# Kernel optimization log

Measured on AMD Instinct MI355X. Metric: run time of the kernel, lower is better.

Reference implementation:

```python
import jax, jax.numpy as jnp
import numpy as np

N_FFT = 2048
HOP = 441
WIN_SIZE = 7
PAD = WIN_SIZE // 2
NP_WIN = WIN_SIZE * WIN_SIZE
COV_NORM = NP_WIN / (NP_WIN - 1.0)  # sample covariance, skimage default
DATA_RANGE = 2.0  # skimage float dtype_range (-1,1)
C1 = (0.01 * DATA_RANGE) ** 2
C2 = (0.03 * DATA_RANGE) ** 2
EPS = 1e-8

# periodic hann window (librosa fftbins=True)
_HANN = 0.5 - 0.5 * np.cos(2.0 * np.pi * np.arange(N_FFT) / N_FFT)


def wav_to_spectrogram(x):
    # x: [B, C, S] -> magnitude spectrogram [B, C, T, F]
    pad = N_FFT // 2
    xp = jnp.pad(x, ((0, 0), (0, 0), (pad, pad)), mode='reflect')  # torch 'reflect'
    L = xp.shape[-1]
    n_frames = (L - N_FFT) // HOP + 1
    idx = jnp.arange(n_frames)[:, None] * HOP + jnp.arange(N_FFT)[None, :]
    frames = xp[..., idx] * jnp.asarray(_HANN, xp.dtype)  # [B,C,T,N_FFT]
    spec = jnp.fft.rfft(frames, axis=-1)
    mag = jnp.sqrt(jnp.maximum(spec.real ** 2 + spec.imag ** 2, EPS))
    return mag


def _umean_last(x):
    # 1D uniform mean filter (size 7) along last axis, scipy 'reflect' boundary
    xp = jnp.pad(x, [(0, 0)] * (x.ndim - 1) + [(PAD, PAD)], mode='symmetric')
    cs = jnp.cumsum(xp, axis=-1)
    zero = jnp.zeros(cs.shape[:-1] + (1,), cs.dtype)
    cs = jnp.concatenate([zero, cs], axis=-1)
    return (cs[..., WIN_SIZE:] - cs[..., :-WIN_SIZE]) / WIN_SIZE


def umean2d(x):
    # separable 7x7 uniform filter over last two axes
    x = _umean_last(x)
    x = jnp.swapaxes(_umean_last(jnp.swapaxes(x, -1, -2)), -1, -2)
    return x


def ssim_map_mean(X, Y):
    ux, uy = umean2d(X), umean2d(Y)
    uxx, uyy, uxy = umean2d(X * X), umean2d(Y * Y), umean2d(X * Y)
    vx = COV_NORM * (uxx - ux * ux)
    vy = COV_NORM * (uyy - uy * uy)
    vxy = COV_NORM * (uxy - ux * uy)
    S = ((2 * ux * uy + C1) * (2 * vxy + C2)) / ((ux * ux + uy * uy + C1) * (vx + vy + C2))
    # crop pad on each side (skimage) then mean over the spatial map
    return jnp.mean(S[..., PAD:-PAD, PAD:-PAD], axis=(-2, -1))


def setup_inputs() -> dict:
    key = jax.random.key(0)
    k1, k2 = jax.random.split(key)
    B, C, S = 32, 2, 176400
    output = jax.random.normal(k1, (B, C, S), dtype=jnp.float32)
    target = jax.random.normal(k2, (B, C, S), dtype=jnp.float32)
    return {"output": output, "target": target}


def reference(output, target):
    so = wav_to_spectrogram(output)
    st = wav_to_spectrogram(target)
    res = ssim_map_mean(so, st)  # [B, C]
    return res[..., None, None]  # [B, C, 1, 1]
```

## Files before the change

kernel.cpp:

```cpp
#include <hip/hip_runtime.h>
#include <math.h>

#ifndef M_PI
#define M_PI 3.14159265358979323846
#endif

constexpr int S_LEN    = 176400;
constexpr int NFFT     = 2048;
constexpr int NC       = 1024;
constexpr int HOP_     = 441;
constexpr int T_FRAMES = 401;
constexpr int F_BINS   = 1025;
constexpr int F_STRIDE = 1028;
constexpr int N_CH     = 64;
constexpr float EPS_   = 1e-8f;
constexpr float C1_    = 0.0004f;
constexpr float C2_    = 0.0036f;
constexpr float COV_NORM_ = 49.0f / 48.0f;

constexpr int WINP_OFF = 0;
constexpr int TG1_OFF  = 2048;
constexpr int TG2_OFF  = 4096;
constexpr int UTW_OFF  = 4224;
constexpr int SPEC_OFF = 6400;
constexpr int RPB_     = 10;
constexpr int N_CHUNKS = 40;

#define WAVE_SYNC() asm volatile("s_waitcnt lgkmcnt(0)" ::: "memory")

__device__ __forceinline__ float2 cadd(float2 a, float2 b){ return make_float2(a.x+b.x, a.y+b.y); }
__device__ __forceinline__ float2 csub(float2 a, float2 b){ return make_float2(a.x-b.x, a.y-b.y); }
__device__ __forceinline__ float2 cmul(float2 a, float2 b){ return make_float2(a.x*b.x-a.y*b.y, a.x*b.y+a.y*b.x); }
__device__ __forceinline__ float2 mulnegi(float2 v){ return make_float2(v.y, -v.x); }

__device__ __constant__ float2 W16C[10] = {
    { 1.0f, 0.0f},
    { 0.92387953251128674f, -0.38268343236508978f},
    { 0.70710678118654752f, -0.70710678118654752f},
    { 0.38268343236508978f, -0.92387953251128674f},
    { 0.0f, -1.0f},
    {-0.38268343236508978f, -0.92387953251128674f},
    {-0.70710678118654752f, -0.70710678118654752f},
    {-0.92387953251128674f, -0.38268343236508978f},
    {-1.0f, 0.0f},
    {-0.92387953251128674f,  0.38268343236508978f},
};

__device__ __forceinline__ void fft16(float2 (&r)[16]) {
    float2 C[4][4];
    #pragma unroll
    for (int m2 = 0; m2 < 4; ++m2) {
        float2 u0 = r[m2], u1 = r[4+m2], u2 = r[8+m2], u3 = r[12+m2];
        float2 t0 = cadd(u0,u2), t1 = csub(u0,u2), t2 = cadd(u1,u3), t3 = csub(u1,u3);
        C[0][m2] = cadd(t0,t2);
        C[1][m2] = cadd(t1, mulnegi(t3));
        C[2][m2] = csub(t0,t2);
        C[3][m2] = csub(t1, mulnegi(t3));
    }
    #pragma unroll
    for (int a = 0; a < 4; ++a) {
        float2 u0 = C[a][0];
        float2 u1 = (a == 0) ? C[a][1] : cmul(C[a][1], W16C[a]);
        float2 u2 = (a == 0) ? C[a][2] : cmul(C[a][2], W16C[2*a]);
        float2 u3 = (a == 0) ? C[a][3] : cmul(C[a][3], W16C[3*a]);
        float2 t0 = cadd(u0,u2), t1 = csub(u0,u2), t2 = cadd(u1,u3), t3 = csub(u1,u3);
        r[a]      = cadd(t0,t2);
        r[a+4]    = cadd(t1, mulnegi(t3));
        r[a+8]    = csub(t0,t2);
        r[a+12]   = csub(t1, mulnegi(t3));
    }
}

__global__ __launch_bounds__(256) void init_tables_kernel(float* __restrict__ ws, float* __restrict__ out) {
    const int idx = blockIdx.x * 256 + threadIdx.x;
    if (idx < 64) out[idx] = 0.0f;
    if (idx < 1024) {
        float w0 = 0.5f - 0.5f * cosf((float)(2.0 * M_PI / NFFT) * (float)(2*idx));
        float w1 = 0.5f - 0.5f * cosf((float)(2.0 * M_PI / NFFT) * (float)(2*idx+1));
        ws[WINP_OFF + 2*idx]   = w0;
        ws[WINP_OFF + 2*idx+1] = w1;
    }
    if (idx < 1024) {
        int k1 = idx >> 6, L = idx & 63;
        float ang = -2.0f * (float)M_PI * (float)(L * k1) / (float)NC;
        float s, c; sincosf(ang, &s, &c);
        ws[TG1_OFF + 2*idx] = c; ws[TG1_OFF + 2*idx+1] = s;
    }
    if (idx < 64) {
        int k2 = idx >> 2, n3 = idx & 3;
        float ang = -2.0f * (float)M_PI * (float)(n3 * k2) / 64.0f;
        float s, c; sincosf(ang, &s, &c);
        ws[TG2_OFF + 2*idx] = c; ws[TG2_OFF + 2*idx+1] = s;
    }
    if (idx < F_BINS) {
        float ang = -(float)M_PI * (float)idx / (float)NC;
        float s, c; sincosf(ang, &s, &c);
        ws[UTW_OFF + 2*idx] = c; ws[UTW_OFF + 2*idx+1] = s;
    }
}

__global__ __launch_bounds__(256) void stft_mag_kernel(
    const float* __restrict__ x0, const float* __restrict__ x1,
    float* __restrict__ ws, int ch0, int nch, int swizzle)
{
    __shared__ float2 lds[4][1024];

    const int tid  = threadIdx.x;
    const int wave = tid >> 6;
    const int L    = tid & 63;

    int ch, pair;
    if (swizzle) {
        int g = blockIdx.x;
        int xcd = g & 7;
        int s = g >> 3;
        int cl = s & 7;
        pair = s >> 3;
        ch = ch0 + xcd * 8 + cl;
    } else {
        pair = blockIdx.x;
        ch = ch0 + blockIdx.y;
    }
    const int which = wave >> 1;
    const int t = 2 * pair + (wave & 1);
    if (t > 400) return;

    const float* __restrict__ xin = (which ? x1 : x0) + (size_t)ch * S_LEN;
    const float2* __restrict__ winp = (const float2*)(ws + WINP_OFF);
    const float2* __restrict__ tg1  = (const float2*)(ws + TG1_OFF);
    const float2* __restrict__ tg2  = (const float2*)(ws + TG2_OFF);
    const float2* __restrict__ utw  = (const float2*)(ws + UTW_OFF);
    float2* B = lds[wave];

    float2 r[16];
    const int base = t * HOP_ - 1024;
    #pragma unroll
    for (int j = 0; j < 16; ++j) {
        const int s0 = base + 128 * j;
        const int i0 = s0 + 2 * L;
        float2 wp = winp[(j << 6) + L];
        float a, b;
        if (s0 >= 0 && s0 + 128 <= S_LEN) {
            a = xin[i0]; b = xin[i0 + 1];
        } else {
            int ia = i0;     ia = (ia < 0) ? -ia : ia; ia = (ia >= S_LEN) ? 2*S_LEN-2-ia : ia;
            int ib = i0 + 1; ib = (ib < 0) ? -ib : ib; ib = (ib >= S_LEN) ? 2*S_LEN-2-ib : ib;
            a = xin[ia]; b = xin[ib];
        }
        r[j] = make_float2(a * wp.x, b * wp.y);
    }

    fft16(r);
    #pragma unroll
    for (int k1 = 0; k1 < 16; ++k1) {
        float2 v = (k1 == 0) ? r[0] : cmul(r[k1], tg1[(k1 << 6) + L]);
        B[(L << 4) + (k1 ^ (L & 15))] = v;
    }
    WAVE_SYNC();

    {
        const int k1 = L & 15, n3 = L >> 4;
        float2 s[16];
        #pragma unroll
        for (int n2 = 0; n2 < 16; ++n2) {
            int lr = (n2 << 2) + n3;
            s[n2] = B[(lr << 4) + (k1 ^ (lr & 15))];
        }
        fft16(s);
        #pragma unroll
        for (int k2 = 1; k2 < 16; ++k2) s[k2] = cmul(s[k2], tg2[(k2 << 2) + n3]);
        WAVE_SYNC();
        #pragma unroll
        for (int k2 = 0; k2 < 16; ++k2) B[(k2 << 6) + L] = s[k2];
    }
    WAVE_SYNC();

    {
        const int g4 = L >> 4, k1b = L & 15;
        float2 D[4][4];
        #pragma unroll
        for (int rr = 0; rr < 4; ++rr)
            #pragma unroll
            for (int n3 = 0; n3 < 4; ++n3)
                D[rr][n3] = B[(g4 << 8) + (rr << 6) + (n3 << 4) + k1b];
        WAVE_SYNC();
        #pragma unroll
        for (int rr = 0; rr < 4; ++rr) {
            float2 e0 = cadd(D[rr][0], D[rr][2]);
            float2 e1 = csub(D[rr][0], D[rr][2]);
            float2 e2 = cadd(D[rr][1], D[rr][3]);
            float2 e3 = csub(D[rr][1], D[rr][3]);
            int kb = k1b + (g4 << 6) + (rr << 4);
            B[kb]       = cadd(e0, e2);
            B[kb + 256] = cadd(e1, mulnegi(e3));
            B[kb + 512] = csub(e0, e2);
            B[kb + 768] = csub(e1, mulnegi(e3));
        }
    }
    WAVE_SYNC();

    {
        float* __restrict__ sout =
            ws + SPEC_OFF + ((size_t)which * nch + (size_t)(ch - ch0)) * (size_t)T_FRAMES * F_STRIDE
                          + (size_t)t * F_STRIDE;
        #pragma unroll
        for (int j = 0; j < 17; ++j) {
            int m = (j << 6) + L;
            if (j < 16 || L == 0) {
                float2 Zr = B[m & 1023];
                float2 Zn = B[(1024 - m) & 1023];
                float Ex = 0.5f * (Zr.x + Zn.x);
                float Ey = 0.5f * (Zr.y - Zn.y);
                float Ox = 0.5f * (Zr.y + Zn.y);
                float Oy = 0.5f * (Zn.x - Zr.x);
                float2 wu = utw[m];
                float Xx = Ex + wu.x * Ox - wu.y * Oy;
                float Xy = Ey + wu.x * Oy + wu.y * Ox;
                sout[m] = sqrtf(fmaxf(Xx * Xx + Xy * Xy, EPS_));
            }
        }
    }
}

__global__ __launch_bounds__(256) void ssim_kernel(
    const float* __restrict__ ws, float* __restrict__ out,
    int ch0, int nch)
{
    __shared__ float csx[1284], csy[1284], csxx[1284], csyy[1284], csxy[1284];
    __shared__ double red[256];

    const int tid = threadIdx.x;
    const int cg  = blockIdx.y;
    const int ch  = ch0 + cg;
    const float* __restrict__ spec = ws + SPEC_OFF;
    const size_t per_ch = (size_t)T_FRAMES * F_STRIDE;
    const float* __restrict__ X = spec + (size_t)cg * per_ch;
    const float* __restrict__ Y = spec + ((size_t)nch + cg) * per_ch;

    const int t_begin = 3 + blockIdx.x * RPB_;
    const int t_end_  = min(t_begin + RPB_, T_FRAMES - 3);

    const int fv = tid << 2;
    const bool last = (tid == 255);
    const float inv49 = 1.0f / 49.0f;
    double acc = 0.0;

    float sx[4] = {0,0,0,0}, sy[4] = {0,0,0,0}, sxx[4] = {0,0,0,0},
          syy[4] = {0,0,0,0}, sxy[4] = {0,0,0,0};
    float s5[5] = {0,0,0,0,0};

    for (int rr = t_begin - 3; rr < t_begin + 3; ++rr) {
        float4 xv = *(const float4*)(X + (size_t)rr * F_STRIDE + fv);
        float4 yv = *(const float4*)(Y + (size_t)rr * F_STRIDE + fv);
        float xa[4] = {xv.x, xv.y, xv.z, xv.w}, ya[4] = {yv.x, yv.y, yv.z, yv.w};
        #pragma unroll
        for (int c = 0; c < 4; ++c) {
            sx[c] += xa[c]; sy[c] += ya[c];
            sxx[c] += xa[c]*xa[c]; syy[c] += ya[c]*ya[c]; sxy[c] += xa[c]*ya[c];
        }
        if (last) {
            float xe = X[(size_t)rr * F_STRIDE + 1024];
            float ye = Y[(size_t)rr * F_STRIDE + 1024];
            s5[0] += xe; s5[1] += ye; s5[2] += xe*xe; s5[3] += ye*ye; s5[4] += xe*ye;
        }
    }

    float4 ax, ay, bx, by; float a5x=0, a5y=0, b5x=0, b5y=0;
    ax = *(const float4*)(X + (size_t)(t_begin + 3) * F_STRIDE + fv);
    ay = *(const float4*)(Y + (size_t)(t_begin + 3) * F_STRIDE + fv);
    bx = *(const float4*)(X + (size_t)(t_begin - 3) * F_STRIDE + fv);
    by = *(const float4*)(Y + (size_t)(t_begin - 3) * F_STRIDE + fv);
    if (last) {
        a5x = X[(size_t)(t_begin + 3) * F_STRIDE + 1024];
        a5y = Y[(size_t)(t_begin + 3) * F_STRIDE + 1024];
        b5x = X[(size_t)(t_begin - 3) * F_STRIDE + 1024];
        b5y = Y[(size_t)(t_begin - 3) * F_STRIDE + 1024];
    }

    const int fo = 3 + (tid << 2);

    for (int t = t_begin; t < t_end_; ++t) {
        {
            float xa[4] = {ax.x, ax.y, ax.z, ax.w}, ya[4] = {ay.x, ay.y, ay.z, ay.w};
            #pragma unroll
            for (int c = 0; c < 4; ++c) {
                sx[c] += xa[c]; sy[c] += ya[c];
                sxx[c] += xa[c]*xa[c]; syy[c] += ya[c]*ya[c]; sxy[c] += xa[c]*ya[c];
                int p = 5 * tid + c;
                csx[p] = sx[c]; csy[p] = sy[c];
                csxx[p] = sxx[c]; csyy[p] = syy[c]; csxy[p] = sxy[c];
            }
            if (last) {
                s5[0] += a5x; s5[1] += a5y; s5[2] += a5x*a5x; s5[3] += a5y*a5y; s5[4] += a5x*a5y;
                csx[1280] = s5[0]; csy[1280] = s5[1];
                csxx[1280] = s5[2]; csyy[1280] = s5[3]; csxy[1280] = s5[4];
            }
        }
        __syncthreads();

        {
            float xa[4] = {bx.x, bx.y, bx.z, bx.w}, ya[4] = {by.x, by.y, by.z, by.w};
            #pragma unroll
            for (int c = 0; c < 4; ++c) {
                sx[c] -= xa[c]; sy[c] -= ya[c];
                sxx[c] -= xa[c]*xa[c]; syy[c] -= ya[c]*ya[c]; sxy[c] -= xa[c]*ya[c];
            }
            if (last) {
                s5[0] -= b5x; s5[1] -= b5y; s5[2] -= b5x*b5x; s5[3] -= b5y*b5y; s5[4] -= b5x*b5y;
            }
        }
        if (t + 1 < t_end_) {
            ax = *(const float4*)(X + (size_t)(t + 4) * F_STRIDE + fv);
            ay = *(const float4*)(Y + (size_t)(t + 4) * F_STRIDE + fv);
            bx = *(const float4*)(X + (size_t)(t - 2) * F_STRIDE + fv);
            by = *(const float4*)(Y + (size_t)(t - 2) * F_STRIDE + fv);
            if (last) {
                a5x = X[(size_t)(t + 4) * F_STRIDE + 1024];
                a5y = Y[(size_t)(t + 4) * F_STRIDE + 1024];
                b5x = X[(size_t)(t - 2) * F_STRIDE + 1024];
                b5y = Y[(size_t)(t - 2) * F_STRIDE + 1024];
            }
        }

        if (tid < 255) {
            float tx[10], ty[10], txx[10], tyy[10], txy[10];
            #pragma unroll
            for (int d = 0; d < 10; ++d) {
                int p = 5 * tid + d + (d >> 2);
                tx[d] = csx[p]; ty[d] = csy[p];
                txx[d] = csxx[p]; tyy[d] = csyy[p]; txy[d] = csxy[p];
            }
            float wx  = tx[0]+tx[1]+tx[2]+tx[3]+tx[4]+tx[5]+tx[6];
            float wy  = ty[0]+ty[1]+ty[2]+ty[3]+ty[4]+ty[5]+ty[6];
            float wxx = txx[0]+txx[1]+txx[2]+txx[3]+txx[4]+txx[5]+txx[6];
            float wyy = tyy[0]+tyy[1]+tyy[2]+tyy[3]+tyy[4]+tyy[5]+tyy[6];
            float wxy = txy[0]+txy[1]+txy[2]+txy[3]+txy[4]+txy[5]+txy[6];
            #pragma unroll
            for (int c = 0; c < 4; ++c) {
                if (fo + c <= 1021) {
                    float ux  = wx * inv49, uy  = wy * inv49;
                    float uxx = wxx * inv49, uyy = wyy * inv49, uxy = wxy * inv49;
                    float vx  = COV_NORM_ * (uxx - ux * ux);
                    float vy  = COV_NORM_ * (uyy - uy * uy);
                    float vxy = COV_NORM_ * (uxy - ux * uy);
                    float Sv = ((2.f * ux * uy + C1_) * (2.f * vxy + C2_)) /
                               ((ux * ux + uy * uy + C1_) * (vx + vy + C2_));
                    acc += (double)Sv;
                }
                if (c < 3) {
                    wx  += tx[c+7]  - tx[c];
                    wy  += ty[c+7]  - ty[c];
                    wxx += txx[c+7] - txx[c];
                    wyy += tyy[c+7] - tyy[c];
                    wxy += txy[c+7] - txy[c];
                }
            }
        }
        __syncthreads();
    }

    red[tid] = acc;
    __syncthreads();
    for (int off = 128; off > 0; off >>= 1) {
        if (tid < off) red[tid] += red[tid + off];
        __syncthreads();
    }
    if (tid == 0) {
        atomicAdd(&out[ch], (float)(red[0] / (395.0 * 1019.0)));
    }
}

extern "C" void kernel_launch(void* const* d_in, const int* in_sizes, int n_in,
                              void* d_out, int out_size, void* d_ws, size_t ws_size,
                              hipStream_t stream) {
    const float* x0 = (const float*)d_in[0];
    const float* x1 = (const float*)d_in[1];
    float* out = (float*)d_out;
    float* ws  = (float*)d_ws;

    const size_t table_bytes  = (size_t)SPEC_OFF * sizeof(float);
    const size_t per_ch_bytes = (size_t)2 * T_FRAMES * F_STRIDE * sizeof(float);
    int G = (int)((ws_size - table_bytes) / per_ch_bytes);
    if (G > N_CH) G = N_CH;
    if (G < 1)    G = 1;

    init_tables_kernel<<<dim3(16), dim3(256), 0, stream>>>(ws, out);

    for (int ch0 = 0; ch0 < N_CH; ch0 += G) {
        const int nch = (N_CH - ch0 < G) ? (N_CH - ch0) : G;

        if (nch == 64) {
            stft_mag_kernel<<<dim3(201 * 64), dim3(256), 0, stream>>>(x0, x1, ws, ch0, nch, 1);
        } else {
            stft_mag_kernel<<<dim3(201, nch), dim3(256), 0, stream>>>(x0, x1, ws, ch0, nch, 0);
        }

        dim3 g2(N_CHUNKS, nch);
        ssim_kernel<<<g2, 256, 0, stream>>>(ws, out, ch0, nch);
    }
}
```

Baseline: 395.7 us.

## Store spectrogram in fp16, halve STFT LDS, exploit conjugate symmetry in output

```diff
diff --git a/kernel.cpp b/kernel.cpp
--- a/kernel.cpp
+++ b/kernel.cpp
@@ -4,6 +4,8 @@
 #ifndef M_PI
 #define M_PI 3.14159265358979323846
 #endif
+
+typedef _Float16 half_t;
 
 constexpr int S_LEN    = 176400;
 constexpr int NFFT     = 2048;
@@ -11,7 +13,7 @@
 constexpr int HOP_     = 441;
 constexpr int T_FRAMES = 401;
 constexpr int F_BINS   = 1025;
-constexpr int F_STRIDE = 1028;
+constexpr int F_STRIDE_H = 1032;
 constexpr int N_CH     = 64;
 constexpr float EPS_   = 1e-8f;
 constexpr float C1_    = 0.0004f;
@@ -99,30 +101,29 @@
     }
 }
 
-__global__ __launch_bounds__(256) void stft_mag_kernel(
+__global__ __launch_bounds__(128, 6) void stft_mag_kernel(
     const float* __restrict__ x0, const float* __restrict__ x1,
     float* __restrict__ ws, int ch0, int nch, int swizzle)
 {
-    __shared__ float2 lds[4][1024];
+    __shared__ float ldsf[2][1088];
 
     const int tid  = threadIdx.x;
     const int wave = tid >> 6;
     const int L    = tid & 63;
 
-    int ch, pair;
+    int ch, pair, which;
     if (swizzle) {
         int g = blockIdx.x;
-        int xcd = g & 7;
-        int s = g >> 3;
-        int cl = s & 7;
-        pair = s >> 3;
-        ch = ch0 + xcd * 8 + cl;
+        ch    = ch0 + (g & 7) * 8 + ((g >> 3) & 7);
+        which = (g >> 6) & 1;
+        pair  = g >> 7;
     } else {
-        pair = blockIdx.x;
-        ch = ch0 + blockIdx.y;
-    }
-    const int which = wave >> 1;
-    const int t = 2 * pair + (wave & 1);
+        int bx = blockIdx.x;
+        which = bx / 201;
+        pair  = bx - which * 201;
+        ch    = ch0 + blockIdx.y;
+    }
+    const int t = 2 * pair + wave;
     if (t > 400) return;
 
     const float* __restrict__ xin = (which ? x1 : x0) + (size_t)ch * S_LEN;
@@ -130,7 +131,7 @@
     const float2* __restrict__ tg1  = (const float2*)(ws + TG1_OFF);
     const float2* __restrict__ tg2  = (const float2*)(ws + TG2_OFF);
     const float2* __restrict__ utw  = (const float2*)(ws + UTW_OFF);
-    float2* B = lds[wave];
+    float* B = ldsf[wave];
 
     float2 r[16];
     const int base = t * HOP_ - 1024;
@@ -152,74 +153,129 @@
 
     fft16(r);
     #pragma unroll
-    for (int k1 = 0; k1 < 16; ++k1) {
-        float2 v = (k1 == 0) ? r[0] : cmul(r[k1], tg1[(k1 << 6) + L]);
-        B[(L << 4) + (k1 ^ (L & 15))] = v;
-    }
-    WAVE_SYNC();
-
+    for (int k1 = 1; k1 < 16; ++k1) r[k1] = cmul(r[k1], tg1[(k1 << 6) + L]);
+
+    const int k1t = L & 15, n3t = L >> 4;
+    const int offA = 17 * n3t + k1t;
+    float sre[16], sim_[16];
     {
-        const int k1 = L & 15, n3 = L >> 4;
-        float2 s[16];
-        #pragma unroll
-        for (int n2 = 0; n2 < 16; ++n2) {
-            int lr = (n2 << 2) + n3;
-            s[n2] = B[(lr << 4) + (k1 ^ (lr & 15))];
-        }
-        fft16(s);
-        #pragma unroll
-        for (int k2 = 1; k2 < 16; ++k2) s[k2] = cmul(s[k2], tg2[(k2 << 2) + n3]);
-        WAVE_SYNC();
-        #pragma unroll
-        for (int k2 = 0; k2 < 16; ++k2) B[(k2 << 6) + L] = s[k2];
-    }
-    WAVE_SYNC();
-
+        const int wbase = 17 * L;
+        #pragma unroll
+        for (int k1 = 0; k1 < 16; ++k1) B[wbase + k1] = r[k1].x;
+        WAVE_SYNC();
+        #pragma unroll
+        for (int n2 = 0; n2 < 16; ++n2) sre[n2] = B[68 * n2 + offA];
+        WAVE_SYNC();
+        #pragma unroll
+        for (int k1 = 0; k1 < 16; ++k1) B[wbase + k1] = r[k1].y;
+        WAVE_SYNC();
+        #pragma unroll
+        for (int n2 = 0; n2 < 16; ++n2) sim_[n2] = B[68 * n2 + offA];
+        WAVE_SYNC();
+    }
+
+    float2 s[16];
+    #pragma unroll
+    for (int n2 = 0; n2 < 16; ++n2) s[n2] = make_float2(sre[n2], sim_[n2]);
+    fft16(s);
+    #pragma unroll
+    for (int k2 = 1; k2 < 16; ++k2) s[k2] = cmul(s[k2], tg2[(k2 << 2) + n3t]);
+
+    const int g4 = L >> 4, k1b = L & 15;
+    const int base3 = 272 * g4 + k1b;
+    float dre[16], dim_[16];
     {
-        const int g4 = L >> 4, k1b = L & 15;
-        float2 D[4][4];
+        #pragma unroll
+        for (int k2 = 0; k2 < 16; ++k2) B[68 * k2 + L] = s[k2].x;
+        WAVE_SYNC();
         #pragma unroll
         for (int rr = 0; rr < 4; ++rr)
             #pragma unroll
-            for (int n3 = 0; n3 < 4; ++n3)
-                D[rr][n3] = B[(g4 << 8) + (rr << 6) + (n3 << 4) + k1b];
-        WAVE_SYNC();
-        #pragma unroll
-        for (int rr = 0; rr < 4; ++rr) {
-            float2 e0 = cadd(D[rr][0], D[rr][2]);
-            float2 e1 = csub(D[rr][0], D[rr][2]);
-            float2 e2 = cadd(D[rr][1], D[rr][3]);
-            float2 e3 = csub(D[rr][1], D[rr][3]);
-            int kb = k1b + (g4 << 6) + (rr << 4);
-            B[kb]       = cadd(e0, e2);
-            B[kb + 256] = cadd(e1, mulnegi(e3));
-            B[kb + 512] = csub(e0, e2);
-            B[kb + 768] = csub(e1, mulnegi(e3));
-        }
-    }
-    WAVE_SYNC();
-
+            for (int n3 = 0; n3 < 4; ++n3) dre[4*rr+n3] = B[base3 + 68*rr + 16*n3];
+        WAVE_SYNC();
+        #pragma unroll
+        for (int k2 = 0; k2 < 16; ++k2) B[68 * k2 + L] = s[k2].y;
+        WAVE_SYNC();
+        #pragma unroll
+        for (int rr = 0; rr < 4; ++rr)
+            #pragma unroll
+            for (int n3 = 0; n3 < 4; ++n3) dim_[4*rr+n3] = B[base3 + 68*rr + 16*n3];
+        WAVE_SYNC();
+    }
+
+    float2 o[16];
+    #pragma unroll
+    for (int rr = 0; rr < 4; ++rr) {
+        float2 D0 = make_float2(dre[4*rr+0], dim_[4*rr+0]);
+        float2 D1 = make_float2(dre[4*rr+1], dim_[4*rr+1]);
+        float2 D2 = make_float2(dre[4*rr+2], dim_[4*rr+2]);
+        float2 D3 = make_float2(dre[4*rr+3], dim_[4*rr+3]);
+        float2 e0 = cadd(D0, D2), e1 = csub(D0, D2);
+        float2 e2 = cadd(D1, D3), e3 = csub(D1, D3);
+        o[4*rr+0] = cadd(e0, e2);
+        o[4*rr+1] = cadd(e1, mulnegi(e3));
+        o[4*rr+2] = csub(e0, e2);
+        o[4*rr+3] = csub(e1, mulnegi(e3));
+    }
+
+    const int kb0 = k1b + (g4 << 6);
+    float zr_re[8], zn_re[8], zr_im[8], zn_im[8];
+    float z5x, z5y;
     {
-        float* __restrict__ sout =
-            ws + SPEC_OFF + ((size_t)which * nch + (size_t)(ch - ch0)) * (size_t)T_FRAMES * F_STRIDE
-                          + (size_t)t * F_STRIDE;
-        #pragma unroll
-        for (int j = 0; j < 17; ++j) {
-            int m = (j << 6) + L;
-            if (j < 16 || L == 0) {
-                float2 Zr = B[m & 1023];
-                float2 Zn = B[(1024 - m) & 1023];
-                float Ex = 0.5f * (Zr.x + Zn.x);
-                float Ey = 0.5f * (Zr.y - Zn.y);
-                float Ox = 0.5f * (Zr.y + Zn.y);
-                float Oy = 0.5f * (Zn.x - Zr.x);
-                float2 wu = utw[m];
-                float Xx = Ex + wu.x * Ox - wu.y * Oy;
-                float Xy = Ey + wu.x * Oy + wu.y * Ox;
-                sout[m] = sqrtf(fmaxf(Xx * Xx + Xy * Xy, EPS_));
-            }
-        }
-    }
+        #pragma unroll
+        for (int rr = 0; rr < 4; ++rr)
+            #pragma unroll
+            for (int k3 = 0; k3 < 4; ++k3) B[kb0 + (rr << 4) + (k3 << 8)] = o[4*rr+k3].x;
+        WAVE_SYNC();
+        #pragma unroll
+        for (int j = 0; j < 8; ++j) {
+            zr_re[j] = B[(j << 6) + L];
+            zn_re[j] = B[(1024 - (j << 6) - L) & 1023];
+        }
+        z5x = B[512];
+        WAVE_SYNC();
+        #pragma unroll
+        for (int rr = 0; rr < 4; ++rr)
+            #pragma unroll
+            for (int k3 = 0; k3 < 4; ++k3) B[kb0 + (rr << 4) + (k3 << 8)] = o[4*rr+k3].y;
+        WAVE_SYNC();
+        #pragma unroll
+        for (int j = 0; j < 8; ++j) {
+            zr_im[j] = B[(j << 6) + L];
+            zn_im[j] = B[(1024 - (j << 6) - L) & 1023];
+        }
+        z5y = B[512];
+    }
+
+    half_t* __restrict__ sout =
+        (half_t*)(ws + SPEC_OFF)
+        + ((size_t)which * nch + (size_t)(ch - ch0)) * (size_t)T_FRAMES * F_STRIDE_H
+        + (size_t)t * F_STRIDE_H;
+    #pragma unroll
+    for (int j = 0; j < 8; ++j) {
+        const int m = (j << 6) + L;
+        float Ex = 0.5f * (zr_re[j] + zn_re[j]);
+        float Ey = 0.5f * (zr_im[j] - zn_im[j]);
+        float Ox = 0.5f * (zr_im[j] + zn_im[j]);
+        float Oy = 0.5f * (zn_re[j] - zr_re[j]);
+        float2 wu = utw[m];
+        float Xx = Ex + wu.x * Ox - wu.y * Oy;
+        float Xy = Ey + wu.x * Oy + wu.y * Ox;
+        sout[m] = (half_t)sqrtf(fmaxf(Xx * Xx + Xy * Xy, EPS_));
+        float Xx2 = Ex - wu.x * Ox + wu.y * Oy;
+        float Xy2 = -Ey + wu.x * Oy + wu.y * Ox;
+        sout[1024 - m] = (half_t)sqrtf(fmaxf(Xx2 * Xx2 + Xy2 * Xy2, EPS_));
+    }
+    if (L == 0) {
+        sout[512] = (half_t)sqrtf(fmaxf(z5x * z5x + z5y * z5y, EPS_));
+    }
+}
+
+__device__ __forceinline__ float4 load4h(const half_t* __restrict__ p) {
+    uint2 u = *(const uint2*)p;
+    union { unsigned v; half_t h[2]; } a, b;
+    a.v = u.x; b.v = u.y;
+    return make_float4((float)a.h[0], (float)a.h[1], (float)b.h[0], (float)b.h[1]);
 }
 
 __global__ __launch_bounds__(256) void ssim_kernel(
@@ -232,10 +288,10 @@
     const int tid = threadIdx.x;
     const int cg  = blockIdx.y;
     const int ch  = ch0 + cg;
-    const float* __restrict__ spec = ws + SPEC_OFF;
-    const size_t per_ch = (size_t)T_FRAMES * F_STRIDE;
-    const float* __restrict__ X = spec + (size_t)cg * per_ch;
-    const float* __restrict__ Y = spec + ((size_t)nch + cg) * per_ch;
+    const half_t* __restrict__ spec = (const half_t*)(ws + SPEC_OFF);
+    const size_t per_ch = (size_t)T_FRAMES * F_STRIDE_H;
+    const half_t* __restrict__ X = spec + (size_t)cg * per_ch;
+    const half_t* __restrict__ Y = spec + ((size_t)nch + cg) * per_ch;
 
     const int t_begin = 3 + blockIdx.x * RPB_;
     const int t_end_  = min(t_begin + RPB_, T_FRAMES - 3);
@@ -250,8 +306,8 @@
     float s5[5] = {0,0,0,0,0};
 
     for (int rr = t_begin - 3; rr < t_begin + 3; ++rr) {
-        float4 xv = *(const float4*)(X + (size_t)rr * F_STRIDE + fv);
-        float4 yv = *(const float4*)(Y + (size_t)rr * F_STRIDE + fv);
+        float4 xv = load4h(X + (size_t)rr * F_STRIDE_H + fv);
+        float4 yv = load4h(Y + (size_t)rr * F_STRIDE_H + fv);
         float xa[4] = {xv.x, xv.y, xv.z, xv.w}, ya[4] = {yv.x, yv.y, yv.z, yv.w};
         #pragma unroll
         for (int c = 0; c < 4; ++c) {
@@ -259,22 +315,22 @@
             sxx[c] += xa[c]*xa[c]; syy[c] += ya[c]*ya[c]; sxy[c] += xa[c]*ya[c];
         }
         if (last) {
-            float xe = X[(size_t)rr * F_STRIDE + 1024];
-            float ye = Y[(size_t)rr * F_STRIDE + 1024];
+            float xe = (float)X[(size_t)rr * F_STRIDE_H + 1024];
+            float ye = (float)Y[(size_t)rr * F_STRIDE_H + 1024];
             s5[0] += xe; s5[1] += ye; s5[2] += xe*xe; s5[3] += ye*ye; s5[4] += xe*ye;
         }
     }
 
     float4 ax, ay, bx, by; float a5x=0, a5y=0, b5x=0, b5y=0;
-    ax = *(const float4*)(X + (size_t)(t_begin + 3) * F_STRIDE + fv);
-    ay = *(const float4*)(Y + (size_t)(t_begin + 3) * F_STRIDE + fv);
-    bx = *(const float4*)(X + (size_t)(t_begin - 3) * F_STRIDE + fv);
-    by = *(const float4*)(Y + (size_t)(t_begin - 3) * F_STRIDE + fv);
+    ax = load4h(X + (size_t)(t_begin + 3) * F_STRIDE_H + fv);
+    ay = load4h(Y + (size_t)(t_begin + 3) * F_STRIDE_H + fv);
+    bx = load4h(X + (size_t)(t_begin - 3) * F_STRIDE_H + fv);
+    by = load4h(Y + (size_t)(t_begin - 3) * F_STRIDE_H + fv);
     if (last) {
-        a5x = X[(size_t)(t_begin + 3) * F_STRIDE + 1024];
-        a5y = Y[(size_t)(t_begin + 3) * F_STRIDE + 1024];
-        b5x = X[(size_t)(t_begin - 3) * F_STRIDE + 1024];
-        b5y = Y[(size_t)(t_begin - 3) * F_STRIDE + 1024];
+        a5x = (float)X[(size_t)(t_begin + 3) * F_STRIDE_H + 1024];
+        a5y = (float)Y[(size_t)(t_begin + 3) * F_STRIDE_H + 1024];
+        b5x = (float)X[(size_t)(t_begin - 3) * F_STRIDE_H + 1024];
+        b5y = (float)Y[(size_t)(t_begin - 3) * F_STRIDE_H + 1024];
     }
 
     const int fo = 3 + (tid << 2);
@@ -310,15 +366,15 @@
             }
         }
         if (t + 1 < t_end_) {
-            ax = *(const float4*)(X + (size_t)(t + 4) * F_STRIDE + fv);
-            ay = *(const float4*)(Y + (size_t)(t + 4) * F_STRIDE + fv);
-            bx = *(const float4*)(X + (size_t)(t - 2) * F_STRIDE + fv);
-            by = *(const float4*)(Y + (size_t)(t - 2) * F_STRIDE + fv);
+            ax = load4h(X + (size_t)(t + 4) * F_STRIDE_H + fv);
+            ay = load4h(Y + (size_t)(t + 4) * F_STRIDE_H + fv);
+            bx = load4h(X + (size_t)(t - 2) * F_STRIDE_H + fv);
+            by = load4h(Y + (size_t)(t - 2) * F_STRIDE_H + fv);
             if (last) {
-                a5x = X[(size_t)(t + 4) * F_STRIDE + 1024];
-                a5y = Y[(size_t)(t + 4) * F_STRIDE + 1024];
-                b5x = X[(size_t)(t - 2) * F_STRIDE + 1024];
-                b5y = Y[(size_t)(t - 2) * F_STRIDE + 1024];
+                a5x = (float)X[(size_t)(t + 4) * F_STRIDE_H + 1024];
+                a5y = (float)Y[(size_t)(t + 4) * F_STRIDE_H + 1024];
+                b5x = (float)X[(size_t)(t - 2) * F_STRIDE_H + 1024];
+                b5y = (float)Y[(size_t)(t - 2) * F_STRIDE_H + 1024];
             }
         }
 
@@ -379,7 +435,7 @@
     float* ws  = (float*)d_ws;
 
     const size_t table_bytes  = (size_t)SPEC_OFF * sizeof(float);
-    const size_t per_ch_bytes = (size_t)2 * T_FRAMES * F_STRIDE * sizeof(float);
+    const size_t per_ch_bytes = (size_t)2 * T_FRAMES * F_STRIDE_H * sizeof(half_t);
     int G = (int)((ws_size - table_bytes) / per_ch_bytes);
     if (G > N_CH) G = N_CH;
     if (G < 1)    G = 1;
@@ -390,9 +446,9 @@
         const int nch = (N_CH - ch0 < G) ? (N_CH - ch0) : G;
 
         if (nch == 64) {
-            stft_mag_kernel<<<dim3(201 * 64), dim3(256), 0, stream>>>(x0, x1, ws, ch0, nch, 1);
+            stft_mag_kernel<<<dim3(201 * 128), dim3(128), 0, stream>>>(x0, x1, ws, ch0, nch, 1);
         } else {
-            stft_mag_kernel<<<dim3(201, nch), dim3(256), 0, stream>>>(x0, x1, ws, ch0, nch, 0);
+            stft_mag_kernel<<<dim3(402, nch), dim3(128), 0, stream>>>(x0, x1, ws, ch0, nch, 0);
         }
 
         dim3 g2(N_CHUNKS, nch);
```

Result: slower. 436.5 us (+10.3%).
